# Performance work log

Hardware: AMD Instinct MI355X
Metric: run time of the kernel (lower is better)

The kernel has to match this reference:

```python
import jax, jax.numpy as jnp
import numpy as np

NUM_GRAPHS = 512
NODES_PER_GRAPH = 200  # == N_rois
EDGES_PER_GRAPH = 3200  # avg degree 16
N_ROIS = 200
HIDDEN = 64
OUT = 2


def setup_inputs() -> dict:
    key = jax.random.key(0)
    ks = jax.random.split(key, 7)
    N = NUM_GRAPHS * NODES_PER_GRAPH
    E = NUM_GRAPHS * EDGES_PER_GRAPH
    x = jax.random.normal(ks[0], (N, N_ROIS), dtype=jnp.float32)
    # edges sampled within each graph's node block
    base = jnp.repeat(jnp.arange(NUM_GRAPHS, dtype=jnp.int64) * NODES_PER_GRAPH, EDGES_PER_GRAPH)
    local = jax.random.randint(ks[1], (2, E), 0, NODES_PER_GRAPH, dtype=jnp.int64)
    edge_index = local + base[None, :]
    batch = jnp.arange(N, dtype=jnp.int64) // NODES_PER_GRAPH
    conv_w = jax.random.normal(ks[2], (N_ROIS, HIDDEN), dtype=jnp.float32) * 0.1
    conv_b = jax.random.normal(ks[3], (HIDDEN,), dtype=jnp.float32) * 0.1
    lin_w = jax.random.normal(ks[4], (HIDDEN, OUT), dtype=jnp.float32) * 0.1
    lin_b = jax.random.normal(ks[5], (OUT,), dtype=jnp.float32) * 0.1
    return {"x": x, "edge_index": edge_index, "batch": batch,
            "conv_w": conv_w, "conv_b": conv_b, "lin_w": lin_w, "lin_b": lin_b}


def reference(x, edge_index, batch, conv_w, conv_b, lin_w, lin_b):
    N = x.shape[0]
    # GCNConv: linear transform first (N_rois -> hidden), then normalized aggregation
    h = x @ conv_w  # [N, H]
    loops = jnp.arange(N, dtype=edge_index.dtype)
    src = jnp.concatenate([edge_index[0], loops])  # add self-loops (PyG default)
    dst = jnp.concatenate([edge_index[1], loops])
    deg = jax.ops.segment_sum(jnp.ones_like(dst, dtype=h.dtype), dst, num_segments=N)
    dinv = jnp.where(deg > 0, jax.lax.rsqrt(deg), jnp.zeros_like(deg))
    norm = dinv[src] * dinv[dst]  # D^-1/2 (A+I) D^-1/2 edge weights
    agg = jax.ops.segment_sum(h[src] * norm[:, None], dst, num_segments=N) + conv_b
    hr = jax.nn.relu(agg)
    x_pool = jax.ops.segment_max(hr, batch, num_segments=NUM_GRAPHS)  # [G, H]
    out = x_pool @ lin_w + lin_b  # [G, OUT]
    return out, x_pool
```

## Files before the change

kernel.cpp:

```cpp
#include <hip/hip_runtime.h>

#define NUM_GRAPHS 512
#define NPG 200
#define EPG 3200
#define NROIS 200
#define HID 64
#define OUTC 2
#define APITCH 232
#define HPITCH 232
#define XPITCH 40
#define WIMG_ELEMS (7 * 4 * 2 * 64 * 8)
#define WS_NEEDED ((size_t)WIMG_ELEMS * 2)

typedef short v8s __attribute__((ext_vector_type(8)));
typedef float v4f __attribute__((ext_vector_type(4)));

__device__ __forceinline__ unsigned bf16_rne(float f) {
  unsigned u = __float_as_uint(f);
  return (u + 0x7fffu + ((u >> 16) & 1u)) >> 16;
}

__global__ void prep_wimg(const float* __restrict__ cw, unsigned short* __restrict__ wimg) {
  int idx = blockIdx.x * 256 + threadIdx.x;
  if (idx >= WIMG_ELEMS) return;
  int i    = idx & 7;
  int lane = (idx >> 3) & 63;
  int hl   = (idx >> 9) & 1;
  int nt   = (idx >> 10) & 3;
  int kt   = idx >> 12;
  int k  = kt * 32 + (lane >> 4) * 8 + i;
  int ch = nt * 16 + (lane & 15);
  float f = (k < NROIS) ? cw[k * HID + ch] : 0.f;
  unsigned hi = bf16_rne(f);
  float lo = f - __uint_as_float(hi << 16);
  wimg[idx] = hl ? (unsigned short)(__float_as_uint(lo) >> 16) : (unsigned short)hi;
}

struct __align__(16) SmemU {
  unsigned char adj[208 * APITCH];
  union {
    struct { unsigned short xhi[NPG * XPITCH];
             unsigned short xlo[NPG * XPITCH]; } g1;
    unsigned short hpTl[HID * HPITCH];
  } u;
  float dinv[NPG];
  int pool[HID];
};

__device__ __forceinline__ void xload(float4* xf, const float* __restrict__ x,
                                      int base, int c0, int tid) {
  #pragma unroll
  for (int r = 0; r < 4; ++r) {
    int idx = tid + r * 512;
    int node = idx >> 3, f4 = idx & 7;
    int col = c0 + f4 * 4;
    if (idx < 1600 && col + 4 <= NROIS)
      xf[r] = *(const float4*)(x + (size_t)(base + node) * NROIS + col);
    else
      xf[r] = make_float4(0.f, 0.f, 0.f, 0.f);
  }
}

__device__ __forceinline__ void xwrite(SmemU& s, const float4* xf, int tid) {
  #pragma unroll
  for (int r = 0; r < 4; ++r) {
    int idx = tid + r * 512;
    if (idx < 1600) {
      int node = idx >> 3, f4 = idx & 7;
      const float ff[4] = {xf[r].x, xf[r].y, xf[r].z, xf[r].w};
      unsigned hh[4], ll[4];
      #pragma unroll
      for (int e = 0; e < 4; ++e) {
        unsigned uu = __float_as_uint(ff[e]);
        hh[e] = uu >> 16;
        float lo = ff[e] - __uint_as_float(hh[e] << 16);
        ll[e] = __float_as_uint(lo) >> 16;
      }
      uint2 ph = {hh[0] | (hh[1] << 16), hh[2] | (hh[3] << 16)};
      uint2 pl = {ll[0] | (ll[1] << 16), ll[2] | (ll[3] << 16)};
      *(uint2*)&s.u.g1.xhi[node * XPITCH + f4 * 4] = ph;
      *(uint2*)&s.u.g1.xlo[node * XPITCH + f4 * 4] = pl;
    }
  }
}

__global__ __launch_bounds__(512, 4)
void gcn_fused3(const float* __restrict__ x,
                const int* __restrict__ ei,
                const unsigned short* __restrict__ wimg,
                const float* __restrict__ cb,
                const float* __restrict__ lw,
                const float* __restrict__ lb,
                float* __restrict__ out,
                int Etot) {
  __shared__ SmemU s;
  const int g = blockIdx.x;
  const int tid = threadIdx.x;
  const int base = g * NPG;
  const int ebase = g * EPG;
  const int lane = tid & 63;
  const int w = __builtin_amdgcn_readfirstlane(tid >> 6);
  const int ml = tid & 15;
  const int q  = (tid >> 4) & 3;

  float4 xf[4];
  xload(xf, x, base, 0, tid);
  int esrc[7], edst[7];
  #pragma unroll
  for (int r = 0; r < 7; ++r) {
    int e = tid + r * 512;
    esrc[r] = -1; edst[r] = 0;
    if (e < EPG) {
      esrc[r] = ei[ebase + e] - base;
      edst[r] = ei[Etot + ebase + e] - base;
    }
  }
  {
    uint4* z = (uint4*)s.adj;
    const uint4 z4 = {0u, 0u, 0u, 0u};
    #pragma unroll
    for (int i = 0; i < 6; ++i) {
      int idx = tid + i * 512;
      if (idx < (208 * APITCH) / 16) z[idx] = z4;
    }
    if (tid < HID) s.pool[tid] = 0;
  }
  __syncthreads();

  {
    unsigned* adjW = (unsigned*)s.adj;
    #pragma unroll
    for (int r = 0; r < 7; ++r) {
      if (esrc[r] >= 0) {
        int idx = edst[r] * APITCH + esrc[r];
        atomicAdd(&adjW[idx >> 2], 1u << ((idx & 3) * 8));
      }
    }
    if (tid < NPG) {
      int idx = tid * APITCH + tid;
      atomicAdd(&adjW[idx >> 2], 1u << ((idx & 3) * 8));
    }
  }
  xwrite(s, xf, tid);
  __syncthreads();

  int mts[2];
  mts[0] = w;
  mts[1] = (w < 5) ? 8 + w : -1;

  v4f acc[2][4];
  #pragma unroll
  for (int a = 0; a < 2; ++a)
    #pragma unroll
    for (int b = 0; b < 4; ++b)
      acc[a][b] = (v4f){0.f, 0.f, 0.f, 0.f};

  for (int kt = 0; kt < 7; ++kt) {
    float4 xfn[4];
    if (kt < 6) xload(xfn, x, base, (kt + 1) * 32, tid);

    v8s whi[4], wlo[4];
    #pragma unroll
    for (int nt = 0; nt < 4; ++nt) {
      const unsigned short* pw = wimg + (size_t)(((kt * 4 + nt) * 2) * 64 + lane) * 8;
      whi[nt] = *(const v8s*)pw;
      wlo[nt] = *(const v8s*)(pw + 64 * 8);
    }
    #pragma unroll
    for (int mi = 0; mi < 2; ++mi) {
      if (mts[mi] >= 0) {
        const int node = mts[mi] * 16 + ml;
        const int nrd = (node < NPG) ? node : 0;
        const v8s xh = *(const v8s*)&s.u.g1.xhi[nrd * XPITCH + q * 8];
        const v8s xl = *(const v8s*)&s.u.g1.xlo[nrd * XPITCH + q * 8];
        #pragma unroll
        for (int nt = 0; nt < 4; ++nt) {
          acc[mi][nt] = __builtin_amdgcn_mfma_f32_16x16x32_bf16(whi[nt], xl, acc[mi][nt], 0, 0, 0);
          acc[mi][nt] = __builtin_amdgcn_mfma_f32_16x16x32_bf16(wlo[nt], xh, acc[mi][nt], 0, 0, 0);
          acc[mi][nt] = __builtin_amdgcn_mfma_f32_16x16x32_bf16(whi[nt], xh, acc[mi][nt], 0, 0, 0);
        }
      }
    }
    __syncthreads();
    if (kt < 6) {
      xwrite(s, xfn, tid);
      __syncthreads();
    }
  }

  if (tid < NPG) {
    const unsigned* ap = (const unsigned*)s.adj + tid * (APITCH / 4);
    unsigned ssum = 0;
    #pragma unroll 2
    for (int j = 0; j < APITCH / 4; ++j)
      ssum += (ap[j] * 0x01010101u) >> 24;
    s.dinv[tid] = rsqrtf((float)ssum);
  }
  {
    int ch = tid >> 3, grp = tid & 7;
    *(uint2*)&s.u.hpTl[ch * HPITCH + 200 + grp * 4] = (uint2){0u, 0u};
  }
  __syncthreads();

  #pragma unroll
  for (int mi = 0; mi < 2; ++mi) {
    if (mts[mi] >= 0) {
      const int node = mts[mi] * 16 + ml;
      if (node < NPG) {
        const float dv = s.dinv[node];
        #pragma unroll
        for (int nt = 0; nt < 4; ++nt) {
          #pragma unroll
          for (int r = 0; r < 4; ++r) {
            const int ch = nt * 16 + q * 4 + r;
            s.u.hpTl[ch * HPITCH + node] = (unsigned short)bf16_rne(dv * acc[mi][nt][r]);
          }
        }
      }
    }
  }
  __syncthreads();

  {
    v4f acc2[2][4];
    #pragma unroll
    for (int a = 0; a < 2; ++a)
      #pragma unroll
      for (int b = 0; b < 4; ++b)
        acc2[a][b] = (v4f){0.f, 0.f, 0.f, 0.f};

    for (int kt = 0; kt < 7; ++kt) {
      const int k0 = kt * 32 + q * 8;

      v8s bf[4];
      #pragma unroll
      for (int nt = 0; nt < 4; ++nt)
        bf[nt] = *(const v8s*)&s.u.hpTl[(nt * 16 + ml) * HPITCH + k0];

      #pragma unroll
      for (int mi = 0; mi < 2; ++mi) {
        if (mts[mi] >= 0) {
          const int row = mts[mi] * 16 + ml;
          const uint2 dd = *(const uint2*)&s.adj[row * APITCH + k0];
          v8s af;
          #pragma unroll
          for (int i = 0; i < 4; ++i) {
            af[i]     = (short)(__float_as_uint((float)((dd.x >> (8 * i)) & 0xffu)) >> 16);
            af[i + 4] = (short)(__float_as_uint((float)((dd.y >> (8 * i)) & 0xffu)) >> 16);
          }
          #pragma unroll
          for (int nt = 0; nt < 4; ++nt)
            acc2[mi][nt] = __builtin_amdgcn_mfma_f32_16x16x32_bf16(af, bf[nt], acc2[mi][nt], 0, 0, 0);
        }
      }
    }

    float cbv[4];
    #pragma unroll
    for (int nt = 0; nt < 4; ++nt) cbv[nt] = cb[nt * 16 + ml];
    float mx[4] = {0.f, 0.f, 0.f, 0.f};
    #pragma unroll
    for (int mi = 0; mi < 2; ++mi) {
      if (mts[mi] >= 0) {
        #pragma unroll
        for (int r = 0; r < 4; ++r) {
          const int row = mts[mi] * 16 + q * 4 + r;
          if (row < NPG) {
            const float dv = s.dinv[row];
            #pragma unroll
            for (int nt = 0; nt < 4; ++nt) {
              float v = fmaxf(fmaf(dv, acc2[mi][nt][r], cbv[nt]), 0.f);
              mx[nt] = fmaxf(mx[nt], v);
            }
          }
        }
      }
    }
    #pragma unroll
    for (int nt = 0; nt < 4; ++nt) {
      mx[nt] = fmaxf(mx[nt], __shfl_xor(mx[nt], 16));
      mx[nt] = fmaxf(mx[nt], __shfl_xor(mx[nt], 32));
    }
    if (q == 0 && (lane >> 5) == 0) {
      #pragma unroll
      for (int nt = 0; nt < 4; ++nt)
        atomicMax(&s.pool[nt * 16 + ml], __float_as_int(mx[nt]));
    }
  }
  __syncthreads();

  if (tid < HID) {
    const float xp = __int_as_float(s.pool[tid]);
    out[NUM_GRAPHS * OUTC + g * HID + tid] = xp;
    float p0 = xp * lw[tid * 2 + 0];
    float p1 = xp * lw[tid * 2 + 1];
    #pragma unroll
    for (int off = 32; off > 0; off >>= 1) {
      p0 += __shfl_down(p0, off);
      p1 += __shfl_down(p1, off);
    }
    if (tid == 0) {
      out[g * OUTC + 0] = p0 + lb[0];
      out[g * OUTC + 1] = p1 + lb[1];
    }
  }
}

struct __align__(16) SmemF {
  unsigned char adj[208 * APITCH];
  unsigned short hpT[HID * HPITCH];
  float dinv[NPG];
  int cnt[NPG];
  int pool[HID];
};

__global__ __launch_bounds__(512, 4)
void gcn_fused_fb(const float* __restrict__ x,
                  const int* __restrict__ ei,
                  const float* __restrict__ cw,
                  const float* __restrict__ cb,
                  const float* __restrict__ lw,
                  const float* __restrict__ lb,
                  float* __restrict__ out,
                  int Etot) {
  __shared__ SmemF s;
  const int g = blockIdx.x;
  const int tid = threadIdx.x;
  const int base = g * NPG;
  const int ebase = g * EPG;
  const int lane = tid & 63;
  const int w = __builtin_amdgcn_readfirstlane(tid >> 6);
  const int ml = tid & 15;
  const int q  = (tid >> 4) & 3;

  {
    uint4* z = (uint4*)&s;
    const uint4 z4 = {0u, 0u, 0u, 0u};
    #pragma unroll
    for (int i = 0; i < 10; ++i) {
      int idx = tid + i * 512;
      if (idx < (208 * APITCH + HID * HPITCH * 2) / 16) z[idx] = z4;
    }
    if (tid < NPG) s.cnt[tid] = 0;
    if (tid < HID) s.pool[tid] = 0;
  }
  __syncthreads();

  int esrc[7], edst[7];
  #pragma unroll
  for (int r = 0; r < 7; ++r) {
    int e = tid + r * 512;
    esrc[r] = -1; edst[r] = 0;
    if (e < EPG) {
      esrc[r] = ei[ebase + e] - base;
      edst[r] = ei[Etot + ebase + e] - base;
      atomicAdd(&s.cnt[edst[r]], 1);
    }
  }
  __syncthreads();

  if (tid < NPG) s.dinv[tid] = rsqrtf((float)(s.cnt[tid] + 1));

  {
    unsigned* adjW = (unsigned*)s.adj;
    #pragma unroll
    for (int r = 0; r < 7; ++r) {
      if (esrc[r] >= 0) {
        int idx = edst[r] * APITCH + esrc[r];
        atomicAdd(&adjW[idx >> 2], 1u << ((idx & 3) * 8));
      }
    }
    if (tid < NPG) {
      int idx = tid * APITCH + tid;
      atomicAdd(&adjW[idx >> 2], 1u << ((idx & 3) * 8));
    }
  }
  __syncthreads();

  {
    int mts[2];
    mts[0] = w;
    mts[1] = (w < 5) ? 8 + w : -1;
    v4f acc[2][4];
    #pragma unroll
    for (int a = 0; a < 2; ++a)
      #pragma unroll
      for (int b = 0; b < 4; ++b)
        acc[a][b] = (v4f){0.f, 0.f, 0.f, 0.f};

    for (int kt = 0; kt < 7; ++kt) {
      const int k0 = kt * 32 + q * 8;
      const bool kok = (k0 < NROIS);
      v8s bhi[4], blo[4];
      #pragma unroll
      for (int nt = 0; nt < 4; ++nt) {
        #pragma unroll
        for (int i = 0; i < 8; ++i) {
          float f = kok ? cw[(k0 + i) * HID + nt * 16 + ml] : 0.f;
          unsigned hb = bf16_rne(f);
          float lo = f - __uint_as_float(hb << 16);
          bhi[nt][i] = (short)hb;
          blo[nt][i] = (short)(__float_as_uint(lo) >> 16);
        }
      }
      #pragma unroll
      for (int mi = 0; mi < 2; ++mi) {
        if (mts[mi] >= 0) {
          const int row = mts[mi] * 16 + ml;
          v8s ahi, alo;
          if (kok && row < NPG) {
            const float* px = x + (size_t)(base + row) * NROIS + k0;
            const float4 f0 = *(const float4*)px;
            const float4 f1 = *(const float4*)(px + 4);
            const float ff[8] = {f0.x, f0.y, f0.z, f0.w, f1.x, f1.y, f1.z, f1.w};
            #pragma unroll
            for (int i = 0; i < 8; ++i) {
              unsigned u = __float_as_uint(ff[i]);
              unsigned hb = u >> 16;
              float lo = ff[i] - __uint_as_float(hb << 16);
              ahi[i] = (short)hb;
              alo[i] = (short)(__float_as_uint(lo) >> 16);
            }
          } else {
            #pragma unroll
            for (int i = 0; i < 8; ++i) { ahi[i] = 0; alo[i] = 0; }
          }
          #pragma unroll
          for (int nt = 0; nt < 4; ++nt) {
            acc[mi][nt] = __builtin_amdgcn_mfma_f32_16x16x32_bf16(ahi, blo[nt], acc[mi][nt], 0, 0, 0);
            acc[mi][nt] = __builtin_amdgcn_mfma_f32_16x16x32_bf16(alo, bhi[nt], acc[mi][nt], 0, 0, 0);
            acc[mi][nt] = __builtin_amdgcn_mfma_f32_16x16x32_bf16(ahi, bhi[nt], acc[mi][nt], 0, 0, 0);
          }
        }
      }
    }
    #pragma unroll
    for (int mi = 0; mi < 2; ++mi) {
      if (mts[mi] >= 0) {
        #pragma unroll
        for (int r = 0; r < 4; ++r) {
          const int row = mts[mi] * 16 + q * 4 + r;
          if (row < NPG) {
            const float dv = s.dinv[row];
            #pragma unroll
            for (int nt = 0; nt < 4; ++nt)
              s.hpT[(nt * 16 + ml) * HPITCH + row] =
                  (unsigned short)bf16_rne(dv * acc[mi][nt][r]);
          }
        }
      }
    }
  }
  __syncthreads();

  {
    int mts[2];
    mts[0] = w;
    mts[1] = (w < 5) ? 8 + w : -1;
    v4f acc2[2][4];
    #pragma unroll
    for (int a = 0; a < 2; ++a)
      #pragma unroll
      for (int b = 0; b < 4; ++b)
        acc2[a][b] = (v4f){0.f, 0.f, 0.f, 0.f};

    for (int kt = 0; kt < 7; ++kt) {
      const int k0 = kt * 32 + q * 8;
      v8s bf[4];
      #pragma unroll
      for (int nt = 0; nt < 4; ++nt)
        bf[nt] = *(const v8s*)&s.hpT[(nt * 16 + ml) * HPITCH + k0];
      #pragma unroll
      for (int mi = 0; mi < 2; ++mi) {
        if (mts[mi] >= 0) {
          const int row = mts[mi] * 16 + ml;
          const uint2 dd = *(const uint2*)&s.adj[row * APITCH + k0];
          v8s af;
          #pragma unroll
          for (int i = 0; i < 4; ++i) {
            af[i]     = (short)(__float_as_uint((float)((dd.x >> (8 * i)) & 0xffu)) >> 16);
            af[i + 4] = (short)(__float_as_uint((float)((dd.y >> (8 * i)) & 0xffu)) >> 16);
          }
          #pragma unroll
          for (int nt = 0; nt < 4; ++nt)
            acc2[mi][nt] = __builtin_amdgcn_mfma_f32_16x16x32_bf16(af, bf[nt], acc2[mi][nt], 0, 0, 0);
        }
      }
    }

    float cbv[4];
    #pragma unroll
    for (int nt = 0; nt < 4; ++nt) cbv[nt] = cb[nt * 16 + ml];
    float mx[4] = {0.f, 0.f, 0.f, 0.f};
    #pragma unroll
    for (int mi = 0; mi < 2; ++mi) {
      if (mts[mi] >= 0) {
        #pragma unroll
        for (int r = 0; r < 4; ++r) {
          const int row = mts[mi] * 16 + q * 4 + r;
          if (row < NPG) {
            const float dv = s.dinv[row];
            #pragma unroll
            for (int nt = 0; nt < 4; ++nt) {
              float v = fmaxf(fmaf(dv, acc2[mi][nt][r], cbv[nt]), 0.f);
              mx[nt] = fmaxf(mx[nt], v);
            }
          }
        }
      }
    }
    #pragma unroll
    for (int nt = 0; nt < 4; ++nt) {
      mx[nt] = fmaxf(mx[nt], __shfl_xor(mx[nt], 16));
      mx[nt] = fmaxf(mx[nt], __shfl_xor(mx[nt], 32));
    }
    if (q == 0 && (lane >> 5) == 0) {
      #pragma unroll
      for (int nt = 0; nt < 4; ++nt)
        atomicMax(&s.pool[nt * 16 + ml], __float_as_int(mx[nt]));
    }
  }
  __syncthreads();

  if (tid < HID) {
    const float xp = __int_as_float(s.pool[tid]);
    out[NUM_GRAPHS * OUTC + g * HID + tid] = xp;
    float p0 = xp * lw[tid * 2 + 0];
    float p1 = xp * lw[tid * 2 + 1];
    #pragma unroll
    for (int off = 32; off > 0; off >>= 1) {
      p0 += __shfl_down(p0, off);
      p1 += __shfl_down(p1, off);
    }
    if (tid == 0) {
      out[g * OUTC + 0] = p0 + lb[0];
      out[g * OUTC + 1] = p1 + lb[1];
    }
  }
}

extern "C" void kernel_launch(void* const* d_in, const int* in_sizes, int n_in,
                              void* d_out, int out_size, void* d_ws, size_t ws_size,
                              hipStream_t stream) {
  const float* x  = (const float*)d_in[0];
  const int*   ei = (const int*)d_in[1];
  const float* cw = (const float*)d_in[3];
  const float* cb = (const float*)d_in[4];
  const float* lw = (const float*)d_in[5];
  const float* lb = (const float*)d_in[6];
  const int Etot = in_sizes[1] / 2;

  if (ws_size >= WS_NEEDED) {
    unsigned short* wimg = (unsigned short*)d_ws;
    prep_wimg<<<(WIMG_ELEMS + 255) / 256, 256, 0, stream>>>(cw, wimg);
    gcn_fused3<<<NUM_GRAPHS, 512, 0, stream>>>(x, ei, wimg, cb, lw, lb,
                                               (float*)d_out, Etot);
  } else {
    gcn_fused_fb<<<NUM_GRAPHS, 512, 0, stream>>>(x, ei, cw, cb, lw, lb,
                                                 (float*)d_out, Etot);
  }
}
```

Baseline: 151.4 us.

## Double-buffer x tiles in LDS, drop x low-part MFMA, hoist degree computation

After: 150.1 us. Within noise of the previous version (-0.8%).

```diff
diff --git a/kernel.cpp b/kernel.cpp
--- a/kernel.cpp
+++ b/kernel.cpp
@@ -39,8 +39,7 @@
 struct __align__(16) SmemU {
   unsigned char adj[208 * APITCH];
   union {
-    struct { unsigned short xhi[NPG * XPITCH];
-             unsigned short xlo[NPG * XPITCH]; } g1;
+    unsigned short xb[2][NPG * XPITCH];
     unsigned short hpTl[HID * HPITCH];
   } u;
   float dinv[NPG];
@@ -61,31 +60,22 @@
   }
 }
 
-__device__ __forceinline__ void xwrite(SmemU& s, const float4* xf, int tid) {
+__device__ __forceinline__ void xwrite(SmemU& s, int buf, const float4* xf, int tid) {
   #pragma unroll
   for (int r = 0; r < 4; ++r) {
     int idx = tid + r * 512;
     if (idx < 1600) {
       int node = idx >> 3, f4 = idx & 7;
-      const float ff[4] = {xf[r].x, xf[r].y, xf[r].z, xf[r].w};
-      unsigned hh[4], ll[4];
-      #pragma unroll
-      for (int e = 0; e < 4; ++e) {
-        unsigned uu = __float_as_uint(ff[e]);
-        hh[e] = uu >> 16;
-        float lo = ff[e] - __uint_as_float(hh[e] << 16);
-        ll[e] = __float_as_uint(lo) >> 16;
-      }
-      uint2 ph = {hh[0] | (hh[1] << 16), hh[2] | (hh[3] << 16)};
-      uint2 pl = {ll[0] | (ll[1] << 16), ll[2] | (ll[3] << 16)};
-      *(uint2*)&s.u.g1.xhi[node * XPITCH + f4 * 4] = ph;
-      *(uint2*)&s.u.g1.xlo[node * XPITCH + f4 * 4] = pl;
+      unsigned b0 = bf16_rne(xf[r].x), b1 = bf16_rne(xf[r].y);
+      unsigned b2 = bf16_rne(xf[r].z), b3 = bf16_rne(xf[r].w);
+      uint2 p = {b0 | (b1 << 16), b2 | (b3 << 16)};
+      *(uint2*)&s.u.xb[buf][node * XPITCH + f4 * 4] = p;
     }
   }
 }
 
 __global__ __launch_bounds__(512, 4)
-void gcn_fused3(const float* __restrict__ x,
+void gcn_fused4(const float* __restrict__ x,
                 const int* __restrict__ ei,
                 const unsigned short* __restrict__ wimg,
                 const float* __restrict__ cb,
@@ -141,8 +131,21 @@
       atomicAdd(&adjW[idx >> 2], 1u << ((idx & 3) * 8));
     }
   }
-  xwrite(s, xf, tid);
-  __syncthreads();
+  xwrite(s, 0, xf, tid);
+  __syncthreads();
+
+  {
+    int row = tid >> 1, half = tid & 1;
+    if (row < NPG) {
+      const unsigned* ap = (const unsigned*)s.adj + row * (APITCH / 4) + half * 29;
+      unsigned ssum = 0;
+      #pragma unroll 4
+      for (int j = 0; j < 29; ++j)
+        ssum += (ap[j] * 0x01010101u) >> 24;
+      ssum += __shfl_xor((int)ssum, 1);
+      if (half == 0) s.dinv[row] = rsqrtf((float)ssum);
+    }
+  }
 
   int mts[2];
   mts[0] = w;
@@ -171,37 +174,22 @@
       if (mts[mi] >= 0) {
         const int node = mts[mi] * 16 + ml;
         const int nrd = (node < NPG) ? node : 0;
-        const v8s xh = *(const v8s*)&s.u.g1.xhi[nrd * XPITCH + q * 8];
-        const v8s xl = *(const v8s*)&s.u.g1.xlo[nrd * XPITCH + q * 8];
+        const v8s xh = *(const v8s*)&s.u.xb[kt & 1][nrd * XPITCH + q * 8];
         #pragma unroll
         for (int nt = 0; nt < 4; ++nt) {
-          acc[mi][nt] = __builtin_amdgcn_mfma_f32_16x16x32_bf16(whi[nt], xl, acc[mi][nt], 0, 0, 0);
           acc[mi][nt] = __builtin_amdgcn_mfma_f32_16x16x32_bf16(wlo[nt], xh, acc[mi][nt], 0, 0, 0);
           acc[mi][nt] = __builtin_amdgcn_mfma_f32_16x16x32_bf16(whi[nt], xh, acc[mi][nt], 0, 0, 0);
         }
       }
     }
+    if (kt < 6) xwrite(s, (kt + 1) & 1, xfn, tid);
     __syncthreads();
-    if (kt < 6) {
-      xwrite(s, xfn, tid);
-      __syncthreads();
-    }
-  }
-
-  if (tid < NPG) {
-    const unsigned* ap = (const unsigned*)s.adj + tid * (APITCH / 4);
-    unsigned ssum = 0;
-    #pragma unroll 2
-    for (int j = 0; j < APITCH / 4; ++j)
-      ssum += (ap[j] * 0x01010101u) >> 24;
-    s.dinv[tid] = rsqrtf((float)ssum);
-  }
+  }
+
   {
     int ch = tid >> 3, grp = tid & 7;
     *(uint2*)&s.u.hpTl[ch * HPITCH + 200 + grp * 4] = (uint2){0u, 0u};
   }
-  __syncthreads();
-
   #pragma unroll
   for (int mi = 0; mi < 2; ++mi) {
     if (mts[mi] >= 0) {
@@ -553,7 +541,7 @@
   if (ws_size >= WS_NEEDED) {
     unsigned short* wimg = (unsigned short*)d_ws;
     prep_wimg<<<(WIMG_ELEMS + 255) / 256, 256, 0, stream>>>(cw, wimg);
-    gcn_fused3<<<NUM_GRAPHS, 512, 0, stream>>>(x, ei, wimg, cb, lw, lb,
+    gcn_fused4<<<NUM_GRAPHS, 512, 0, stream>>>(x, ei, wimg, cb, lw, lb,
                                                (float*)d_out, Etot);
   } else {
     gcn_fused_fb<<<NUM_GRAPHS, 512, 0, stream>>>(x, ei, cw, cb, lw, lb,
```
